# Optimization experiments

Measured on AMD Instinct MI355X. Metric: run time of the kernel, lower is better.

Reference implementation:

```python
import jax, jax.numpy as jnp
import numpy as np

B, S, F, D = 4, 1024, 8, 512
H = 8
DK = D // H
DF = 2048
ECLIPSE_BOOST = 2.0
LN_EPS = 1e-5


def _layer_norm(x, g, b):
    m = jnp.mean(x, axis=-1, keepdims=True)
    v = jnp.mean(jnp.square(x - m), axis=-1, keepdims=True)
    return (x - m) * jax.lax.rsqrt(v + LN_EPS) * g + b


def setup_inputs() -> dict:
    key = jax.random.key(0)
    ks = jax.random.split(key, 16)
    def lin_w(k, out_d, in_d):
        return jax.random.normal(k, (out_d, in_d), jnp.float32) * (1.0 / np.sqrt(in_d))
    return {
        "x": jax.random.normal(ks[0], (B, S, F, D), jnp.float32),
        "eclipse_mask": jax.random.bernoulli(ks[1], 0.3, (B, S)),
        "wq": lin_w(ks[2], D, D), "bq": jnp.zeros((D,), jnp.float32),
        "wk": lin_w(ks[3], D, D), "bk": jnp.zeros((D,), jnp.float32),
        "wv": lin_w(ks[4], D, D), "bv": jnp.zeros((D,), jnp.float32),
        "wo": lin_w(ks[5], D, D), "bo": jnp.zeros((D,), jnp.float32),
        "w1": lin_w(ks[6], DF, D), "b1": jnp.zeros((DF,), jnp.float32),
        "w2": lin_w(ks[7], D, DF), "b2": jnp.zeros((D,), jnp.float32),
        "g1": jnp.ones((D,), jnp.float32), "be1": jnp.zeros((D,), jnp.float32),
        "g2": jnp.ones((D,), jnp.float32), "be2": jnp.zeros((D,), jnp.float32),
    }


def reference(x, eclipse_mask, wq, bq, wk, bk, wv, bv, wo, bo, w1, b1, w2, b2, g1, be1, g2, be2):
    BF = B * F
    scale = 1.0 / np.sqrt(DK)
    # NOTE: the torch module does x.view(B*F, S, D) on a [B,S,F,D] tensor —
    # a raw memory reshape (NOT a transpose). Replicate exactly.
    xr = x.reshape(BF, S, D)  # [BF, S, D]
    # eclipse_mask [B,S] -> expand over features -> [BF, S] (rows b*F+f share mask[b])
    em = jnp.broadcast_to(eclipse_mask[:, None, :], (B, F, S)).reshape(BF, S)

    def proj(w, b):
        return (xr @ w.T + b).reshape(BF, S, H, DK).transpose(0, 2, 1, 3)  # [BF,H,S,DK]

    Q, K, V = proj(wq, bq), proj(wk, bk), proj(wv, bv)
    scores = jnp.einsum("bhqd,bhkd->bhqk", Q, K) * scale  # [BF,H,S,S]
    boost = jnp.where(em, ECLIPSE_BOOST, 1.0)[:, None, None, :]  # over key positions
    scores = scores * boost
    attn = jax.nn.softmax(scores, axis=-1)
    ctx = jnp.einsum("bhqk,bhkd->bhqd", attn, V)  # [BF,H,S,DK]
    ctx = ctx.transpose(0, 2, 1, 3).reshape(BF, S, D)
    attn_out = (ctx @ wo.T + bo).reshape(B, S, F, D)  # raw reshape back, matches torch

    h = _layer_norm(x + attn_out, g1, be1)
    ff = jax.nn.gelu(h @ w1.T + b1, approximate=False) @ w2.T + b2
    return _layer_norm(h + ff, g2, be2)
```

## Files before the change

kernel.cpp:

```cpp
#include <hip/hip_runtime.h>
#include <math.h>

typedef _Float16 half8 __attribute__((ext_vector_type(8)));
typedef float f32x4 __attribute__((ext_vector_type(4)));
typedef unsigned int u32;

#define AS1 __attribute__((address_space(1)))
#define AS3 __attribute__((address_space(3)))

__device__ __forceinline__ void g2lds16(const void* g, void* l) {
    __builtin_amdgcn_global_load_lds((const AS1 u32*)g, (AS3 u32*)l, 16, 0, 0);
}

__global__ __launch_bounds__(256)
void cvt_all(const float* __restrict__ x, const float* __restrict__ wq,
             const float* __restrict__ wk, const float* __restrict__ wv,
             const float* __restrict__ wo, const float* __restrict__ w1,
             const float* __restrict__ w2, _Float16* __restrict__ xh,
             _Float16* __restrict__ qkvw, _Float16* __restrict__ woh,
             _Float16* __restrict__ w1h, _Float16* __restrict__ w2h)
{
    const int bid = blockIdx.x;
    const float* src; _Float16* dst; int g;
    if (bid < 8192)      { src = x;  dst = xh;            g = bid*256 + threadIdx.x; }
    else if (bid < 8320) { src = wq; dst = qkvw;          g = (bid-8192)*256 + threadIdx.x; }
    else if (bid < 8448) { src = wk; dst = qkvw + 262144; g = (bid-8320)*256 + threadIdx.x; }
    else if (bid < 8576) { src = wv; dst = qkvw + 524288; g = (bid-8448)*256 + threadIdx.x; }
    else if (bid < 8704) { src = wo; dst = woh;           g = (bid-8576)*256 + threadIdx.x; }
    else if (bid < 9216) { src = w1; dst = w1h;           g = (bid-8704)*256 + threadIdx.x; }
    else                 { src = w2; dst = w2h;           g = (bid-9216)*256 + threadIdx.x; }
    const float4* p = (const float4*)src + (size_t)g * 2;
    float4 a = p[0], b = p[1];
    half8 h;
    h[0]=(_Float16)a.x; h[1]=(_Float16)a.y; h[2]=(_Float16)a.z; h[3]=(_Float16)a.w;
    h[4]=(_Float16)b.x; h[5]=(_Float16)b.y; h[6]=(_Float16)b.z; h[7]=(_Float16)b.w;
    *((half8*)dst + g) = h;
}

__global__ __launch_bounds__(256)
void pack_bias(const float* __restrict__ bq, const float* __restrict__ bk,
               const float* __restrict__ bv, float* __restrict__ o)
{
    const int i = blockIdx.x * 256 + threadIdx.x;
    o[i] = i < 512 ? bq[i] : (i < 1024 ? bk[i-512] : bv[i-1024]);
}

template<int MODE>
__global__ __launch_bounds__(256)
void gemm_bt(const _Float16* __restrict__ A, const _Float16* __restrict__ B,
             const float* __restrict__ bias, const float* __restrict__ resf,
             const _Float16* __restrict__ resh, void* __restrict__ Cout,
             int M, int N, int K)
{
    __shared__ __align__(16) _Float16 As[128 * 32];
    __shared__ __align__(16) _Float16 Bs[128 * 32];
    const int tid = threadIdx.x;
    const int lane = tid & 63;
    const int w = tid >> 6;
    const int wm = w >> 1, wn = w & 1;
    const int m0 = blockIdx.y * 128, n0 = blockIdx.x * 128;
    const int lrow = lane & 15;
    const int lk = (lane >> 4) * 8;

    f32x4 acc[4][4];
#pragma unroll
    for (int i = 0; i < 4; ++i)
#pragma unroll
        for (int j = 0; j < 4; ++j) acc[i][j] = (f32x4)0.0f;

    for (int k0 = 0; k0 < K; k0 += 32) {
#pragma unroll
        for (int i = 0; i < 2; ++i) {
            int gbase = i * 256 + w * 64;
            int g = gbase + lane;
            g2lds16(A + (size_t)(m0 + (g >> 2)) * K + k0 + (g & 3) * 8,
                    (char*)As + (size_t)gbase * 16);
            g2lds16(B + (size_t)(n0 + (g >> 2)) * K + k0 + (g & 3) * 8,
                    (char*)Bs + (size_t)gbase * 16);
        }
        __syncthreads();
        half8 af[4], bfr[4];
#pragma unroll
        for (int t = 0; t < 4; ++t) {
            af[t]  = *(const half8*)(As + (wm * 64 + t * 16 + lrow) * 32 + lk);
            bfr[t] = *(const half8*)(Bs + (wn * 64 + t * 16 + lrow) * 32 + lk);
        }
#pragma unroll
        for (int mi = 0; mi < 4; ++mi)
#pragma unroll
            for (int ni = 0; ni < 4; ++ni)
                acc[mi][ni] = __builtin_amdgcn_mfma_f32_16x16x32_f16(af[mi], bfr[ni], acc[mi][ni], 0, 0, 0);
        __syncthreads();
    }

    const int rq = (lane >> 4) * 4;
#pragma unroll
    for (int mi = 0; mi < 4; ++mi) {
#pragma unroll
        for (int ni = 0; ni < 4; ++ni) {
            const int col = n0 + wn * 64 + ni * 16 + lrow;
            const float bv = bias[col];
#pragma unroll
            for (int r = 0; r < 4; ++r) {
                const int row = m0 + wm * 64 + mi * 16 + rq + r;
                const size_t idx = (size_t)row * N + col;
                float v = acc[mi][ni][r] + bv;
                if (MODE == 0) {
                    ((_Float16*)Cout)[idx] = (_Float16)v;
                } else if (MODE == 1) {
                    float t2 = -1.5957691216057308f * v * fmaf(v * v, 0.044715f, 1.0f);
                    float e = __expf(t2);
                    ((_Float16*)Cout)[idx] = (_Float16)(v * __builtin_amdgcn_rcpf(1.0f + e));
                } else if (MODE == 2) {
                    ((float*)Cout)[idx] = v + resf[idx];
                } else {
                    ((float*)Cout)[idx] = v + (float)resh[idx];
                }
            }
        }
    }
}

__global__ __launch_bounds__(256)
void attn_fwd(const _Float16* __restrict__ QKV, const int* __restrict__ mask,
              _Float16* __restrict__ ctx)
{
    constexpr int SQ = 72;
    __shared__ __align__(16) _Float16 Ks[64 * SQ];
    __shared__ __align__(16) _Float16 Vts[64 * SQ];
    __shared__ __align__(16) _Float16 Ps[4][32 * SQ];
    __shared__ float scs[1024];

    const int tid = threadIdx.x;
    const int lane = tid & 63;
    const int w = tid >> 6;
    const int bf = blockIdx.y >> 3;
    const int hh = blockIdx.y & 7;
    const int q0 = blockIdx.x * 128;
    const int lrow = lane & 15;
    const int lq = lane >> 4;

    {
        const int* mrow = mask + (bf >> 3) * 1024;
        const int i = tid * 4;
        int4 mm = *(const int4*)(mrow + i);
        scs[i + 0] = mm.x ? 0.25f : 0.125f;
        scs[i + 1] = mm.y ? 0.25f : 0.125f;
        scs[i + 2] = mm.z ? 0.25f : 0.125f;
        scs[i + 3] = mm.w ? 0.25f : 0.125f;
    }

    half8 qf[2][2];
#pragma unroll
    for (int qi = 0; qi < 2; ++qi) {
        const _Float16* qp = QKV + (size_t)(bf * 1024 + q0 + w * 32 + qi * 16 + lrow) * 1536 + hh * 64 + lq * 8;
        qf[qi][0] = *(const half8*)qp;
        qf[qi][1] = *(const half8*)(qp + 32);
    }

    const _Float16* Kbase = QKV + (size_t)bf * 1024 * 1536 + 512 + hh * 64;
    const _Float16* Vbase = Kbase + 512;

    f32x4 acc[2][4];
#pragma unroll
    for (int qi = 0; qi < 2; ++qi)
#pragma unroll
        for (int d = 0; d < 4; ++d) acc[qi][d] = (f32x4)0.0f;
    float lpart[2][4] = {{0.f,0.f,0.f,0.f},{0.f,0.f,0.f,0.f}};
    _Float16* Pw = &Ps[w][0];

    for (int kt = 0; kt < 1024; kt += 64) {
        __syncthreads();
        {
            const int r = tid >> 3, c = (tid & 7) * 8;
            *(uint4*)&Ks[r * SQ + c]        = *(const uint4*)(Kbase + (size_t)(kt + r) * 1536 + c);
            *(uint4*)&Ks[(r + 32) * SQ + c] = *(const uint4*)(Kbase + (size_t)(kt + r + 32) * 1536 + c);
            const int key = lane, dvb = w * 16;
            const _Float16* vp = Vbase + (size_t)(kt + key) * 1536 + dvb;
            half8 v0 = *(const half8*)vp;
            half8 v1 = *(const half8*)(vp + 8);
#pragma unroll
            for (int j = 0; j < 8; ++j) Vts[(dvb + j) * SQ + key] = v0[j];
#pragma unroll
            for (int j = 0; j < 8; ++j) Vts[(dvb + 8 + j) * SQ + key] = v1[j];
        }
        __syncthreads();

#pragma unroll
        for (int nt = 0; nt < 4; ++nt) {
            half8 kf0 = *(const half8*)(Ks + (nt * 16 + lrow) * SQ + lq * 8);
            half8 kf1 = *(const half8*)(Ks + (nt * 16 + lrow) * SQ + 32 + lq * 8);
            const float sc = scs[kt + nt * 16 + lrow];
#pragma unroll
            for (int qi = 0; qi < 2; ++qi) {
                f32x4 s = (f32x4)0.0f;
                s = __builtin_amdgcn_mfma_f32_16x16x32_f16(qf[qi][0], kf0, s, 0, 0, 0);
                s = __builtin_amdgcn_mfma_f32_16x16x32_f16(qf[qi][1], kf1, s, 0, 0, 0);
#pragma unroll
                for (int r = 0; r < 4; ++r) {
                    float p = __expf(fmaf(s[r], sc, -5.0f));
                    lpart[qi][r] += p;
                    Pw[(qi * 16 + lq * 4 + r) * SQ + nt * 16 + lrow] = (_Float16)p;
                }
            }
        }

        half8 pf[2][2];
#pragma unroll
        for (int qi = 0; qi < 2; ++qi) {
            pf[qi][0] = *(const half8*)(Pw + (qi * 16 + lrow) * SQ + lq * 8);
            pf[qi][1] = *(const half8*)(Pw + (qi * 16 + lrow) * SQ + 32 + lq * 8);
        }
#pragma unroll
        for (int d = 0; d < 4; ++d) {
            half8 vf0 = *(const half8*)(Vts + (d * 16 + lrow) * SQ + lq * 8);
            half8 vf1 = *(const half8*)(Vts + (d * 16 + lrow) * SQ + 32 + lq * 8);
#pragma unroll
            for (int qi = 0; qi < 2; ++qi) {
                acc[qi][d] = __builtin_amdgcn_mfma_f32_16x16x32_f16(pf[qi][0], vf0, acc[qi][d], 0, 0, 0);
                acc[qi][d] = __builtin_amdgcn_mfma_f32_16x16x32_f16(pf[qi][1], vf1, acc[qi][d], 0, 0, 0);
            }
        }
    }

#pragma unroll
    for (int qi = 0; qi < 2; ++qi) {
#pragma unroll
        for (int r = 0; r < 4; ++r) {
            float l = lpart[qi][r];
            l += __shfl_xor(l, 1); l += __shfl_xor(l, 2);
            l += __shfl_xor(l, 4); l += __shfl_xor(l, 8);
            const float inv = 1.0f / l;
            const int row = q0 + w * 32 + qi * 16 + lq * 4 + r;
            _Float16* cp = ctx + ((size_t)bf * 1024 + row) * 512 + hh * 64;
#pragma unroll
            for (int d = 0; d < 4; ++d)
                cp[d * 16 + lrow] = (_Float16)(acc[qi][d][r] * inv);
        }
    }
}

template<int OUTH>
__global__ __launch_bounds__(256)
void ln_fused(const float* __restrict__ X, const float* __restrict__ gma,
              const float* __restrict__ bta, float* __restrict__ outF,
              _Float16* __restrict__ outH)
{
    const int row = blockIdx.x * 4 + (threadIdx.x >> 6);
    const int lane = threadIdx.x & 63;
    const float4* xr = (const float4*)(X + (size_t)row * 512);
    float4 a = xr[lane * 2], c = xr[lane * 2 + 1];
    float s  = a.x + a.y + a.z + a.w + c.x + c.y + c.z + c.w;
    float s2 = a.x * a.x + a.y * a.y + a.z * a.z + a.w * a.w
             + c.x * c.x + c.y * c.y + c.z * c.z + c.w * c.w;
#pragma unroll
    for (int m = 1; m < 64; m <<= 1) { s += __shfl_xor(s, m); s2 += __shfl_xor(s2, m); }
    const float mean = s * (1.0f / 512.0f);
    const float inv = rsqrtf(s2 * (1.0f / 512.0f) - mean * mean + 1e-5f);
    const float4* gp = (const float4*)gma;
    const float4* bp = (const float4*)bta;
    float4 g0 = gp[lane * 2], g1 = gp[lane * 2 + 1];
    float4 b0 = bp[lane * 2], b1 = bp[lane * 2 + 1];
    float4 o0, o1;
    o0.x = (a.x - mean) * inv * g0.x + b0.x; o0.y = (a.y - mean) * inv * g0.y + b0.y;
    o0.z = (a.z - mean) * inv * g0.z + b0.z; o0.w = (a.w - mean) * inv * g0.w + b0.w;
    o1.x = (c.x - mean) * inv * g1.x + b1.x; o1.y = (c.y - mean) * inv * g1.y + b1.y;
    o1.z = (c.z - mean) * inv * g1.z + b1.z; o1.w = (c.w - mean) * inv * g1.w + b1.w;
    if (OUTH) {
        half8 hv;
        hv[0] = (_Float16)o0.x; hv[1] = (_Float16)o0.y; hv[2] = (_Float16)o0.z; hv[3] = (_Float16)o0.w;
        hv[4] = (_Float16)o1.x; hv[5] = (_Float16)o1.y; hv[6] = (_Float16)o1.z; hv[7] = (_Float16)o1.w;
        *((half8*)(outH + (size_t)row * 512) + lane) = hv;
    } else {
        float4* op = (float4*)(outF + (size_t)row * 512);
        op[lane * 2] = o0; op[lane * 2 + 1] = o1;
    }
}

extern "C" void kernel_launch(void* const* d_in, const int* in_sizes, int n_in,
                              void* d_out, int out_size, void* d_ws, size_t ws_size,
                              hipStream_t stream)
{
    const float* x   = (const float*)d_in[0];
    const int* mask  = (const int*)d_in[1];
    const float* wq  = (const float*)d_in[2];  const float* bq  = (const float*)d_in[3];
    const float* wk  = (const float*)d_in[4];  const float* bk  = (const float*)d_in[5];
    const float* wv  = (const float*)d_in[6];  const float* bv  = (const float*)d_in[7];
    const float* wo  = (const float*)d_in[8];  const float* bo  = (const float*)d_in[9];
    const float* w1  = (const float*)d_in[10]; const float* b1  = (const float*)d_in[11];
    const float* w2  = (const float*)d_in[12]; const float* b2  = (const float*)d_in[13];
    const float* g1  = (const float*)d_in[14]; const float* be1 = (const float*)d_in[15];
    const float* g2  = (const float*)d_in[16]; const float* be2 = (const float*)d_in[17];
    float* out = (float*)d_out;

    char* ws = (char*)d_ws;
    _Float16* qkvh = (_Float16*)(ws);
    _Float16* ctxh = (_Float16*)(ws + 100663296);
    _Float16* gh   = (_Float16*)(ws);
    _Float16* xh   = (_Float16*)(ws + 134217728);
    float*    res  = (float*)   (ws + 134217728);
    _Float16* hhb  = (_Float16*)(ws + 201326592);
    float*    biasf= (float*)   (ws + 201326592);
    _Float16* qkvw = (_Float16*)(ws + 234881024);
    _Float16* woh  = (_Float16*)(ws + 236453888);
    _Float16* w1h  = (_Float16*)(ws + 236978176);
    _Float16* w2h  = (_Float16*)(ws + 239075328);

    dim3 blk(256);

    cvt_all<<<9728, blk, 0, stream>>>(x, wq, wk, wv, wo, w1, w2, xh, qkvw, woh, w1h, w2h);
    pack_bias<<<6, blk, 0, stream>>>(bq, bk, bv, biasf);

    gemm_bt<0><<<dim3(12, 256), blk, 0, stream>>>(xh, qkvw, biasf, nullptr, nullptr, qkvh, 32768, 1536, 512);

    attn_fwd<<<dim3(8, 256), blk, 0, stream>>>(qkvh, mask, ctxh);

    gemm_bt<2><<<dim3(4, 256), blk, 0, stream>>>(ctxh, woh, bo, x, nullptr, res, 32768, 512, 512);

    ln_fused<1><<<8192, blk, 0, stream>>>(res, g1, be1, nullptr, hhb);

    gemm_bt<1><<<dim3(16, 256), blk, 0, stream>>>(hhb, w1h, b1, nullptr, nullptr, gh, 32768, 2048, 512);

    gemm_bt<3><<<dim3(4, 256), blk, 0, stream>>>(gh, w2h, b2, nullptr, hhb, res, 32768, 512, 2048);

    ln_fused<0><<<8192, blk, 0, stream>>>(res, g2, be2, out, nullptr);
}
```

Baseline: 701.4 us.

## Write V pre-transposed from QKV GEMM and drop LDS staging in attention

The QKV projection epilogue now writes V into a separate per-head transposed buffer, so attention can load V fragments straight from global memory. K is also read directly from global, which removes the per-tile LDS staging and two block barriers per key tile. The softmax switches to exp2 with log2e folded into the scale constants, the row-sum is computed with an extra MFMA against a ones vector instead of shuffles, the block-to-head mapping is swizzled, and setprio is raised around the PV MFMAs. The risks are scattered 2-byte writes for the transposed V in the GEMM epilogue and uncached global reads of K/V being repeated by each wave.

```diff
diff --git a/kernel.cpp b/kernel.cpp
--- a/kernel.cpp
+++ b/kernel.cpp
@@ -11,6 +11,12 @@
 __device__ __forceinline__ void g2lds16(const void* g, void* l) {
     __builtin_amdgcn_global_load_lds((const AS1 u32*)g, (AS3 u32*)l, 16, 0, 0);
 }
+
+#if __has_builtin(__builtin_amdgcn_exp2f)
+#define EXP2F(x) __builtin_amdgcn_exp2f(x)
+#else
+#define EXP2F(x) exp2f(x)
+#endif
 
 __global__ __launch_bounds__(256)
 void cvt_all(const float* __restrict__ x, const float* __restrict__ wq,
@@ -49,8 +55,8 @@
 __global__ __launch_bounds__(256)
 void gemm_bt(const _Float16* __restrict__ A, const _Float16* __restrict__ B,
              const float* __restrict__ bias, const float* __restrict__ resf,
-             const _Float16* __restrict__ resh, void* __restrict__ Cout,
-             int M, int N, int K)
+             const _Float16* __restrict__ resh, _Float16* __restrict__ vTout,
+             void* __restrict__ Cout, int M, int N, int K)
 {
     __shared__ __align__(16) _Float16 As[128 * 32];
     __shared__ __align__(16) _Float16 Bs[128 * 32];
@@ -106,7 +112,14 @@
                 const size_t idx = (size_t)row * N + col;
                 float v = acc[mi][ni][r] + bv;
                 if (MODE == 0) {
-                    ((_Float16*)Cout)[idx] = (_Float16)v;
+                    if (col < 1024) {
+                        ((_Float16*)Cout)[idx] = (_Float16)v;
+                    } else {
+                        const int dkf = col - 1024;
+                        const size_t tidx = (((size_t)((row >> 10) * 8 + (dkf >> 6))) << 16)
+                                          + ((size_t)(dkf & 63) << 10) + (size_t)(row & 1023);
+                        vTout[tidx] = (_Float16)v;
+                    }
                 } else if (MODE == 1) {
                     float t2 = -1.5957691216057308f * v * fmaf(v * v, 0.044715f, 1.0f);
                     float e = __expf(t2);
@@ -121,22 +134,25 @@
     }
 }
 
-__global__ __launch_bounds__(256)
-void attn_fwd(const _Float16* __restrict__ QKV, const int* __restrict__ mask,
-              _Float16* __restrict__ ctx)
+__global__ __launch_bounds__(256, 4)
+void attn_fwd(const _Float16* __restrict__ QKV, const _Float16* __restrict__ vT,
+              const int* __restrict__ mask, _Float16* __restrict__ ctx)
 {
     constexpr int SQ = 72;
-    __shared__ __align__(16) _Float16 Ks[64 * SQ];
-    __shared__ __align__(16) _Float16 Vts[64 * SQ];
     __shared__ __align__(16) _Float16 Ps[4][32 * SQ];
     __shared__ float scs[1024];
 
     const int tid = threadIdx.x;
     const int lane = tid & 63;
     const int w = tid >> 6;
-    const int bf = blockIdx.y >> 3;
-    const int hh = blockIdx.y & 7;
-    const int q0 = blockIdx.x * 128;
+
+    const int p = blockIdx.y * 8 + blockIdx.x;
+    const int ii = p >> 3;
+    const int headlin = (p & 7) * 32 + (ii >> 3);
+    const int bf = headlin >> 3;
+    const int hh = headlin & 7;
+    const int q0 = (ii & 7) * 128;
+
     const int lrow = lane & 15;
     const int lq = lane >> 4;
 
@@ -144,11 +160,13 @@
         const int* mrow = mask + (bf >> 3) * 1024;
         const int i = tid * 4;
         int4 mm = *(const int4*)(mrow + i);
-        scs[i + 0] = mm.x ? 0.25f : 0.125f;
-        scs[i + 1] = mm.y ? 0.25f : 0.125f;
-        scs[i + 2] = mm.z ? 0.25f : 0.125f;
-        scs[i + 3] = mm.w ? 0.25f : 0.125f;
-    }
+        scs[i + 0] = mm.x ? 0.36067376f : 0.18033688f;
+        scs[i + 1] = mm.y ? 0.36067376f : 0.18033688f;
+        scs[i + 2] = mm.z ? 0.36067376f : 0.18033688f;
+        scs[i + 3] = mm.w ? 0.36067376f : 0.18033688f;
+    }
+    __syncthreads();
+    constexpr float B2 = -7.2134752f;
 
     half8 qf[2][2];
 #pragma unroll
@@ -158,38 +176,32 @@
         qf[qi][1] = *(const half8*)(qp + 32);
     }
 
-    const _Float16* Kbase = QKV + (size_t)bf * 1024 * 1536 + 512 + hh * 64;
-    const _Float16* Vbase = Kbase + 512;
+    const _Float16* Kg = QKV + (size_t)bf * 1024 * 1536 + 512 + hh * 64;
+    const _Float16* Vg = vT + (size_t)(bf * 8 + hh) * 65536;
 
     f32x4 acc[2][4];
 #pragma unroll
     for (int qi = 0; qi < 2; ++qi)
 #pragma unroll
         for (int d = 0; d < 4; ++d) acc[qi][d] = (f32x4)0.0f;
-    float lpart[2][4] = {{0.f,0.f,0.f,0.f},{0.f,0.f,0.f,0.f}};
+    f32x4 acc_l[2] = {(f32x4)0.0f, (f32x4)0.0f};
+    const half8 ones = {(_Float16)1.f,(_Float16)1.f,(_Float16)1.f,(_Float16)1.f,
+                        (_Float16)1.f,(_Float16)1.f,(_Float16)1.f,(_Float16)1.f};
     _Float16* Pw = &Ps[w][0];
 
     for (int kt = 0; kt < 1024; kt += 64) {
-        __syncthreads();
-        {
-            const int r = tid >> 3, c = (tid & 7) * 8;
-            *(uint4*)&Ks[r * SQ + c]        = *(const uint4*)(Kbase + (size_t)(kt + r) * 1536 + c);
-            *(uint4*)&Ks[(r + 32) * SQ + c] = *(const uint4*)(Kbase + (size_t)(kt + r + 32) * 1536 + c);
-            const int key = lane, dvb = w * 16;
-            const _Float16* vp = Vbase + (size_t)(kt + key) * 1536 + dvb;
-            half8 v0 = *(const half8*)vp;
-            half8 v1 = *(const half8*)(vp + 8);
-#pragma unroll
-            for (int j = 0; j < 8; ++j) Vts[(dvb + j) * SQ + key] = v0[j];
-#pragma unroll
-            for (int j = 0; j < 8; ++j) Vts[(dvb + 8 + j) * SQ + key] = v1[j];
-        }
-        __syncthreads();
+        half8 vf[4][2];
+#pragma unroll
+        for (int d = 0; d < 4; ++d)
+#pragma unroll
+            for (int t = 0; t < 2; ++t)
+                vf[d][t] = *(const half8*)(Vg + (size_t)(d * 16 + lrow) * 1024 + kt + t * 32 + lq * 8);
 
 #pragma unroll
         for (int nt = 0; nt < 4; ++nt) {
-            half8 kf0 = *(const half8*)(Ks + (nt * 16 + lrow) * SQ + lq * 8);
-            half8 kf1 = *(const half8*)(Ks + (nt * 16 + lrow) * SQ + 32 + lq * 8);
+            const _Float16* kp = Kg + (size_t)(kt + nt * 16 + lrow) * 1536 + lq * 8;
+            half8 kf0 = *(const half8*)kp;
+            half8 kf1 = *(const half8*)(kp + 32);
             const float sc = scs[kt + nt * 16 + lrow];
 #pragma unroll
             for (int qi = 0; qi < 2; ++qi) {
@@ -197,11 +209,9 @@
                 s = __builtin_amdgcn_mfma_f32_16x16x32_f16(qf[qi][0], kf0, s, 0, 0, 0);
                 s = __builtin_amdgcn_mfma_f32_16x16x32_f16(qf[qi][1], kf1, s, 0, 0, 0);
 #pragma unroll
-                for (int r = 0; r < 4; ++r) {
-                    float p = __expf(fmaf(s[r], sc, -5.0f));
-                    lpart[qi][r] += p;
-                    Pw[(qi * 16 + lq * 4 + r) * SQ + nt * 16 + lrow] = (_Float16)p;
-                }
+                for (int r = 0; r < 4; ++r)
+                    Pw[(qi * 16 + lq * 4 + r) * SQ + nt * 16 + lrow] =
+                        (_Float16)EXP2F(fmaf(s[r], sc, B2));
             }
         }
 
@@ -211,26 +221,27 @@
             pf[qi][0] = *(const half8*)(Pw + (qi * 16 + lrow) * SQ + lq * 8);
             pf[qi][1] = *(const half8*)(Pw + (qi * 16 + lrow) * SQ + 32 + lq * 8);
         }
-#pragma unroll
-        for (int d = 0; d < 4; ++d) {
-            half8 vf0 = *(const half8*)(Vts + (d * 16 + lrow) * SQ + lq * 8);
-            half8 vf1 = *(const half8*)(Vts + (d * 16 + lrow) * SQ + 32 + lq * 8);
+        __builtin_amdgcn_s_setprio(1);
+#pragma unroll
+        for (int d = 0; d < 4; ++d)
 #pragma unroll
             for (int qi = 0; qi < 2; ++qi) {
-                acc[qi][d] = __builtin_amdgcn_mfma_f32_16x16x32_f16(pf[qi][0], vf0, acc[qi][d], 0, 0, 0);
-                acc[qi][d] = __builtin_amdgcn_mfma_f32_16x16x32_f16(pf[qi][1], vf1, acc[qi][d], 0, 0, 0);
+                acc[qi][d] = __builtin_amdgcn_mfma_f32_16x16x32_f16(pf[qi][0], vf[d][0], acc[qi][d], 0, 0, 0);
+                acc[qi][d] = __builtin_amdgcn_mfma_f32_16x16x32_f16(pf[qi][1], vf[d][1], acc[qi][d], 0, 0, 0);
             }
-        }
+#pragma unroll
+        for (int qi = 0; qi < 2; ++qi) {
+            acc_l[qi] = __builtin_amdgcn_mfma_f32_16x16x32_f16(pf[qi][0], ones, acc_l[qi], 0, 0, 0);
+            acc_l[qi] = __builtin_amdgcn_mfma_f32_16x16x32_f16(pf[qi][1], ones, acc_l[qi], 0, 0, 0);
+        }
+        __builtin_amdgcn_s_setprio(0);
     }
 
 #pragma unroll
     for (int qi = 0; qi < 2; ++qi) {
 #pragma unroll
         for (int r = 0; r < 4; ++r) {
-            float l = lpart[qi][r];
-            l += __shfl_xor(l, 1); l += __shfl_xor(l, 2);
-            l += __shfl_xor(l, 4); l += __shfl_xor(l, 8);
-            const float inv = 1.0f / l;
+            const float inv = 1.0f / acc_l[qi][r];
             const int row = q0 + w * 32 + qi * 16 + lq * 4 + r;
             _Float16* cp = ctx + ((size_t)bf * 1024 + row) * 512 + hh * 64;
 #pragma unroll
@@ -299,6 +310,7 @@
     _Float16* gh   = (_Float16*)(ws);
     _Float16* xh   = (_Float16*)(ws + 134217728);
     float*    res  = (float*)   (ws + 134217728);
+    _Float16* vTh  = (_Float16*)(ws + 167772160);
     _Float16* hhb  = (_Float16*)(ws + 201326592);
     float*    biasf= (float*)   (ws + 201326592);
     _Float16* qkvw = (_Float16*)(ws + 234881024);
@@ -311,17 +323,17 @@
     cvt_all<<<9728, blk, 0, stream>>>(x, wq, wk, wv, wo, w1, w2, xh, qkvw, woh, w1h, w2h);
     pack_bias<<<6, blk, 0, stream>>>(bq, bk, bv, biasf);
 
-    gemm_bt<0><<<dim3(12, 256), blk, 0, stream>>>(xh, qkvw, biasf, nullptr, nullptr, qkvh, 32768, 1536, 512);
-
-    attn_fwd<<<dim3(8, 256), blk, 0, stream>>>(qkvh, mask, ctxh);
-
-    gemm_bt<2><<<dim3(4, 256), blk, 0, stream>>>(ctxh, woh, bo, x, nullptr, res, 32768, 512, 512);
+    gemm_bt<0><<<dim3(12, 256), blk, 0, stream>>>(xh, qkvw, biasf, nullptr, nullptr, vTh, qkvh, 32768, 1536, 512);
+
+    attn_fwd<<<dim3(8, 256), blk, 0, stream>>>(qkvh, vTh, mask, ctxh);
+
+    gemm_bt<2><<<dim3(4, 256), blk, 0, stream>>>(ctxh, woh, bo, x, nullptr, nullptr, res, 32768, 512, 512);
 
     ln_fused<1><<<8192, blk, 0, stream>>>(res, g1, be1, nullptr, hhb);
 
-    gemm_bt<1><<<dim3(16, 256), blk, 0, stream>>>(hhb, w1h, b1, nullptr, nullptr, gh, 32768, 2048, 512);
-
-    gemm_bt<3><<<dim3(4, 256), blk, 0, stream>>>(gh, w2h, b2, nullptr, hhb, res, 32768, 512, 2048);
+    gemm_bt<1><<<dim3(16, 256), blk, 0, stream>>>(hhb, w1h, b1, nullptr, nullptr, nullptr, gh, 32768, 2048, 512);
+
+    gemm_bt<3><<<dim3(4, 256), blk, 0, stream>>>(gh, w2h, b2, nullptr, hhb, nullptr, res, 32768, 512, 2048);
 
     ln_fused<0><<<8192, blk, 0, stream>>>(res, g2, be2, out, nullptr);
 }
```

Result: slower. 831.8 us (+18.6%).
